# Performance work log

Measured on AMD Instinct MI355X. Metric: run time of the kernel, lower is better.

Reference implementation:

```python
import jax, jax.numpy as jnp
import numpy as np

B = 4_194_304  # production-scale batch; model itself is tiny


def setup_inputs() -> dict:
    key = jax.random.key(0)
    ks = jax.random.split(key, 8)
    inputs = jax.random.normal(ks[0], (B, 2), dtype=jnp.float32)
    # MLP params, stored as [in, out] (torch Linear uses x @ W.T + b; equivalent math)
    W1 = jax.random.normal(ks[1], (3, 8), dtype=jnp.float32) * (1.0 / np.sqrt(3.0))
    b1 = jax.random.normal(ks[2], (8,), dtype=jnp.float32) * 0.1
    W2 = jax.random.normal(ks[3], (8, 4), dtype=jnp.float32) * (1.0 / np.sqrt(8.0))
    b2 = jax.random.normal(ks[4], (4,), dtype=jnp.float32) * 0.1
    W3 = jax.random.normal(ks[5], (4, 1), dtype=jnp.float32) * (1.0 / np.sqrt(4.0))
    b3 = jax.random.normal(ks[6], (1,), dtype=jnp.float32) * 0.1
    w = jax.random.normal(ks[7], (1,), dtype=jnp.float32)  # weight_param
    return {"inputs": inputs, "W1": W1, "b1": b1, "W2": W2, "b2": b2,
            "W3": W3, "b3": b3, "w": w}


def _quantum_feature(inputs, w):
    # Closed form of: |0> -H-> RY(x0) -> RX(x1) -> RX(w), then <Y>.
    # Bloch: (1,0,0) -RY(x0)-> (cos x0, 0, -sin x0) -RX(x1+w)-> y = sin(x0)*sin(x1+w)
    return jnp.sin(inputs[:, 0:1]) * jnp.sin(inputs[:, 1:2] + w)  # [B, 1]


def reference(inputs, W1, b1, W2, b2, W3, b3, w):
    q_feat = _quantum_feature(inputs, w)              # [B, 1]
    aug = jnp.concatenate([inputs, q_feat], axis=1)   # [B, 3]
    h = jnp.tanh(aug @ W1 + b1)                       # [B, 8]
    h = jnp.tanh(h @ W2 + b2)                         # [B, 4]
    return h @ W3 + b3                                # [B, 1]
```

## Files before the change

kernel.cpp:

```cpp
#include <hip/hip_runtime.h>
#include <math.h>


#define NEG2LOG2E -2.8853900817779268f
#define INV2PI     0.15915494309189535f

__device__ __forceinline__ float sigm2(float x) {
    float t = __builtin_amdgcn_exp2f(x * NEG2LOG2E);
    return __builtin_amdgcn_rcpf(1.0f + t);
}

__global__ __launch_bounds__(256) void qnn_fused_kernel(
    const float* __restrict__ in,
    const float* __restrict__ W1,
    const float* __restrict__ b1,
    const float* __restrict__ W2,
    const float* __restrict__ b2,
    const float* __restrict__ W3,
    const float* __restrict__ b3,
    const float* __restrict__ wq,
    float* __restrict__ out,
    int n)
{
    const float wC = wq[0] * INV2PI;

    float w1[3][8];
#pragma unroll
    for (int i = 0; i < 3; ++i)
#pragma unroll
        for (int j = 0; j < 8; ++j) w1[i][j] = W1[i * 8 + j];
    float bb1[8];
#pragma unroll
    for (int j = 0; j < 8; ++j) bb1[j] = b1[j];

    float w2d[8][4];
    float bb2p[4];
#pragma unroll
    for (int j = 0; j < 4; ++j) {
        float s = 0.0f;
#pragma unroll
        for (int i = 0; i < 8; ++i) {
            float v = W2[i * 4 + j];
            w2d[i][j] = 2.0f * v;
            s += v;
        }
        bb2p[j] = b2[j] - s;
    }

    float w3d[4];
    float s3 = 0.0f;
#pragma unroll
    for (int i = 0; i < 4; ++i) { float v = W3[i]; w3d[i] = 2.0f * v; s3 += v; }
    const float bb3p = b3[0] - s3;

    auto forward = [&](float x0, float x1) -> float {
        float q = __builtin_amdgcn_sinf(x0 * INV2PI)
                * __builtin_amdgcn_sinf(fmaf(x1, INV2PI, wC));
        float r1[8];
#pragma unroll
        for (int j = 0; j < 8; ++j) {
            float acc = fmaf(x0, w1[0][j],
                        fmaf(x1, w1[1][j],
                        fmaf(q,  w1[2][j], bb1[j])));
            r1[j] = sigm2(acc);
        }
        float r2[4];
#pragma unroll
        for (int j = 0; j < 4; ++j) {
            float acc = bb2p[j];
#pragma unroll
            for (int i = 0; i < 8; ++i) acc = fmaf(r1[i], w2d[i][j], acc);
            r2[j] = sigm2(acc);
        }
        float o = bb3p;
#pragma unroll
        for (int i = 0; i < 4; ++i) o = fmaf(r2[i], w3d[i], o);
        return o;
    };

    const int base = (blockIdx.x * blockDim.x + threadIdx.x) * 4;
    if (base + 3 < n) {
        const float4 p0 = *reinterpret_cast<const float4*>(in + 2 * base);
        const float4 p1 = *reinterpret_cast<const float4*>(in + 2 * base + 4);
        float4 o;
        o.x = forward(p0.x, p0.y);
        o.y = forward(p0.z, p0.w);
        o.z = forward(p1.x, p1.y);
        o.w = forward(p1.z, p1.w);
        *reinterpret_cast<float4*>(out + base) = o;
    } else {
        for (int e = 0; e < 4; ++e) {
            int i = base + e;
            if (i < n) out[i] = forward(in[2 * i], in[2 * i + 1]);
        }
    }
}

extern "C" void kernel_launch(void* const* d_in, const int* in_sizes, int n_in,
                              void* d_out, int out_size, void* d_ws, size_t ws_size,
                              hipStream_t stream) {
    const float* in = (const float*)d_in[0];
    const float* W1 = (const float*)d_in[1];
    const float* b1 = (const float*)d_in[2];
    const float* W2 = (const float*)d_in[3];
    const float* b2 = (const float*)d_in[4];
    const float* W3 = (const float*)d_in[5];
    const float* b3 = (const float*)d_in[6];
    const float* wq = (const float*)d_in[7];
    float* out = (float*)d_out;

    const int n = out_size;
    const int threads = 256;
    const int elems_per_block = threads * 4;
    const int blocks = (n + elems_per_block - 1) / elems_per_block;

    hipLaunchKernelGGL(qnn_fused_kernel, dim3(blocks), dim3(threads), 0, stream,
                       in, W1, b1, W2, b2, W3, b3, wq, out, n);
}
```

Before: 100.4 us.

## Pack MLP math into v_pk_fma pairs and share one reciprocal per sigmoid pair

Regroups the hidden-layer neurons into float2 pairs so the layer FMAs can map to packed v_pk_fma_f32 instructions. Each pair of sigmoids now computes both from a single reciprocal, 1/(a*b), which removes one transcendental rcp per pair at the cost of a few extra multiplies. The input loads are also issued before the weight loads so memory latency overlaps the setup work. The risks are extra register pressure and the shuffles needed to broadcast scalars into packed operands, plus a small precision and overflow risk from multiplying the two denominators.

```diff
diff --git a/kernel.cpp b/kernel.cpp
--- a/kernel.cpp
+++ b/kernel.cpp
@@ -5,9 +5,23 @@
 #define NEG2LOG2E -2.8853900817779268f
 #define INV2PI     0.15915494309189535f
 
-__device__ __forceinline__ float sigm2(float x) {
-    float t = __builtin_amdgcn_exp2f(x * NEG2LOG2E);
-    return __builtin_amdgcn_rcpf(1.0f + t);
+typedef float v2f __attribute__((ext_vector_type(2)));
+
+__device__ __forceinline__ v2f pk_fma(v2f a, v2f b, v2f c) {
+    return __builtin_elementwise_fma(a, b, c);
+}
+
+__device__ __forceinline__ v2f sigm2_pair(v2f x) {
+    v2f xm = x * NEG2LOG2E;
+    v2f t;
+    t.x = __builtin_amdgcn_exp2f(xm.x);
+    t.y = __builtin_amdgcn_exp2f(xm.y);
+    v2f a = t + 1.0f;
+    float rd = __builtin_amdgcn_rcpf(a.x * a.y);
+    v2f r;
+    r.x = a.y * rd;
+    r.y = a.x * rd;
+    return r;
 }
 
 __global__ __launch_bounds__(256) void qnn_fused_kernel(
@@ -22,66 +36,88 @@
     float* __restrict__ out,
     int n)
 {
+    const int base = (blockIdx.x * blockDim.x + threadIdx.x) * 4;
+
+    float4 p0, p1;
+    const bool fast = (base + 3 < n);
+    if (fast) {
+        const float4* src = reinterpret_cast<const float4*>(in + 2 * base);
+        p0 = src[0];
+        p1 = src[1];
+    }
+
     const float wC = wq[0] * INV2PI;
 
-    float w1[3][8];
+    v2f w1v[3][4];
 #pragma unroll
     for (int i = 0; i < 3; ++i)
 #pragma unroll
-        for (int j = 0; j < 8; ++j) w1[i][j] = W1[i * 8 + j];
-    float bb1[8];
+        for (int jp = 0; jp < 4; ++jp) {
+            w1v[i][jp].x = W1[i * 8 + 2 * jp];
+            w1v[i][jp].y = W1[i * 8 + 2 * jp + 1];
+        }
+    v2f b1v[4];
 #pragma unroll
-    for (int j = 0; j < 8; ++j) bb1[j] = b1[j];
+    for (int jp = 0; jp < 4; ++jp) { b1v[jp].x = b1[2 * jp]; b1v[jp].y = b1[2 * jp + 1]; }
 
-    float w2d[8][4];
-    float bb2p[4];
+    v2f w2v[8][2];
+    v2f b2v[2];
 #pragma unroll
-    for (int j = 0; j < 4; ++j) {
-        float s = 0.0f;
+    for (int jp = 0; jp < 2; ++jp) {
+        float s0 = 0.0f, s1 = 0.0f;
 #pragma unroll
         for (int i = 0; i < 8; ++i) {
-            float v = W2[i * 4 + j];
-            w2d[i][j] = 2.0f * v;
-            s += v;
+            float vx = W2[i * 4 + 2 * jp];
+            float vy = W2[i * 4 + 2 * jp + 1];
+            w2v[i][jp].x = 2.0f * vx;
+            w2v[i][jp].y = 2.0f * vy;
+            s0 += vx; s1 += vy;
         }
-        bb2p[j] = b2[j] - s;
+        b2v[jp].x = b2[2 * jp] - s0;
+        b2v[jp].y = b2[2 * jp + 1] - s1;
     }
 
-    float w3d[4];
+    v2f w3v[2];
     float s3 = 0.0f;
 #pragma unroll
-    for (int i = 0; i < 4; ++i) { float v = W3[i]; w3d[i] = 2.0f * v; s3 += v; }
+    for (int i = 0; i < 4; ++i) { float v = W3[i]; (i < 2 ? w3v[0] : w3v[1])[i & 1] = 2.0f * v; s3 += v; }
     const float bb3p = b3[0] - s3;
 
     auto forward = [&](float x0, float x1) -> float {
         float q = __builtin_amdgcn_sinf(x0 * INV2PI)
                 * __builtin_amdgcn_sinf(fmaf(x1, INV2PI, wC));
-        float r1[8];
+        v2f x0v = {x0, x0}, x1v = {x1, x1}, qv = {q, q};
+
+        v2f r1[4];
 #pragma unroll
-        for (int j = 0; j < 8; ++j) {
-            float acc = fmaf(x0, w1[0][j],
-                        fmaf(x1, w1[1][j],
-                        fmaf(q,  w1[2][j], bb1[j])));
-            r1[j] = sigm2(acc);
+        for (int jp = 0; jp < 4; ++jp) {
+            v2f acc = pk_fma(x0v, w1v[0][jp],
+                      pk_fma(x1v, w1v[1][jp],
+                      pk_fma(qv,  w1v[2][jp], b1v[jp])));
+            r1[jp] = sigm2_pair(acc);
         }
-        float r2[4];
+
+        v2f r2[2];
 #pragma unroll
-        for (int j = 0; j < 4; ++j) {
-            float acc = bb2p[j];
+        for (int jp = 0; jp < 2; ++jp) {
+            v2f acc = b2v[jp];
 #pragma unroll
-            for (int i = 0; i < 8; ++i) acc = fmaf(r1[i], w2d[i][j], acc);
-            r2[j] = sigm2(acc);
+            for (int ip = 0; ip < 4; ++ip) {
+                v2f rlo = {r1[ip].x, r1[ip].x};
+                v2f rhi = {r1[ip].y, r1[ip].y};
+                acc = pk_fma(rlo, w2v[2 * ip][jp], acc);
+                acc = pk_fma(rhi, w2v[2 * ip + 1][jp], acc);
+            }
+            r2[jp] = sigm2_pair(acc);
         }
-        float o = bb3p;
-#pragma unroll
-        for (int i = 0; i < 4; ++i) o = fmaf(r2[i], w3d[i], o);
-        return o;
+
+        v2f oacc = {bb3p, 0.0f};
+        oacc = pk_fma(r2[0], w3v[0], oacc);
+        oacc = pk_fma(r2[1], w3v[1], oacc);
+        return oacc.x + oacc.y;
     };
 
-    const int base = (blockIdx.x * blockDim.x + threadIdx.x) * 4;
-    if (base + 3 < n) {
-        const float4 p0 = *reinterpret_cast<const float4*>(in + 2 * base);
-        const float4 p1 = *reinterpret_cast<const float4*>(in + 2 * base + 4);
+    if (fast) {
         float4 o;
         o.x = forward(p0.x, p0.y);
         o.y = forward(p0.z, p0.w);
```

New measurement: 98.11 us, median of 2. -2.2%, faster.
